# Kernel tuning notes

Measured on AMD Instinct MI355X. Metric: run time of the kernel, lower is better.

## Reference

```python
import jax, jax.numpy as jnp
import numpy as np
from jax import lax

K = 3  # kernel size
KK = K * K


def _bilinear_gather(img, ys, xs):
    """img: [C, H, W]; ys, xs: [KK, H, W] float sample coords.
    Returns [C, KK, H, W], zero outside the image (torch DCN zero-pad semantics)."""
    C, H, W = img.shape
    y0 = jnp.floor(ys).astype(jnp.int32)
    x0 = jnp.floor(xs).astype(jnp.int32)
    y1, x1 = y0 + 1, x0 + 1
    wy1 = ys - y0.astype(ys.dtype)
    wx1 = xs - x0.astype(xs.dtype)
    wy0, wx0 = 1.0 - wy1, 1.0 - wx1

    def g(yi, xi):
        valid = ((yi >= 0) & (yi < H) & (xi >= 0) & (xi < W)).astype(img.dtype)
        yc = jnp.clip(yi, 0, H - 1)
        xc = jnp.clip(xi, 0, W - 1)
        return img[:, yc, xc] * valid[None]  # [C, KK, H, W]

    return (wy0 * wx0) * g(y0, x0) + (wy0 * wx1) * g(y0, x1) \
         + (wy1 * wx0) * g(y1, x0) + (wy1 * wx1) * g(y1, x1)


def _df_layer(x, w_off, b_off, w):
    """One DFConv2d (modulated DCN, k=3, s=1, d=1, pad=1, groups=1) + ReLU."""
    B, C, H, W = x.shape
    O = w.shape[0]
    # offset/mask conv (standard 3x3, pad 1, with bias)
    om = lax.conv_general_dilated(x, w_off, (1, 1), [(1, 1), (1, 1)],
                                  dimension_numbers=('NCHW', 'OIHW', 'NCHW'))
    om = om + b_off[None, :, None, None]                     # [B, 27, H, W]
    off = om[:, :2 * KK].reshape(B, KK, 2, H, W)             # (dy, dx) per kernel pt
    mask = jax.nn.sigmoid(om[:, 2 * KK:3 * KK])              # [B, KK, H, W]

    ki, kj = jnp.meshgrid(jnp.arange(K), jnp.arange(K), indexing='ij')
    # base sampling grid: y = h - pad + i*dil = h + i - 1
    base_y = jnp.arange(H, dtype=x.dtype)[None, :, None] + (ki.reshape(KK, 1, 1).astype(x.dtype) - 1.0)
    base_x = jnp.arange(W, dtype=x.dtype)[None, None, :] + (kj.reshape(KK, 1, 1).astype(x.dtype) - 1.0)
    ys = base_y + off[:, :, 0]                               # [B, KK, H, W]
    xs = base_x + off[:, :, 1]

    sampled = jax.vmap(_bilinear_gather)(x, ys, xs)          # [B, C, KK, H, W]
    out = jnp.einsum('oik,bikhw->bohw', w.reshape(O, C, KK), sampled * mask[:, None])
    return jax.nn.relu(out)


def setup_inputs() -> dict:
    key = jax.random.key(0)
    ks = jax.random.split(key, 7)
    s = 0.05
    return {
        'x': jax.random.normal(ks[0], (2, 256, 96, 96), dtype=jnp.float32),
        'w_off0': jax.random.normal(ks[1], (27, 256, 3, 3), dtype=jnp.float32) * s,
        'b_off0': jnp.zeros((27,), dtype=jnp.float32),
        'w0': jax.random.normal(ks[2], (256, 256, 3, 3), dtype=jnp.float32) * s,
        'w_off1': jax.random.normal(ks[3], (27, 256, 3, 3), dtype=jnp.float32) * s,
        'b_off1': jnp.zeros((27,), dtype=jnp.float32),
        'w1': jax.random.normal(ks[4], (256, 256, 3, 3), dtype=jnp.float32) * s,
    }


def reference(x, w_off0, b_off0, w0, w_off1, b_off1, w1):
    h = _df_layer(x, w_off0, b_off0, w0)
    h = _df_layer(h, w_off1, b_off1, w1)
    return h
```

## Files before the change

### kernel.cpp

```cpp
#include <hip/hip_runtime.h>
#include <cstdint>
#include <cstddef>


#define KTOT 2304
#define PXB  9216

typedef __attribute__((ext_vector_type(8))) short bf16x8;
typedef __attribute__((ext_vector_type(4))) float f32x4;

static __device__ __forceinline__ unsigned short f2bf(float f) {
    union { float f; unsigned int u; } v; v.f = f;
    unsigned int r = (v.u + 0x7FFFu + ((v.u >> 16) & 1u)) >> 16;
    return (unsigned short)r;
}
static __device__ __forceinline__ float bf2f(unsigned short h) {
    union { unsigned int u; float f; } v; v.u = ((unsigned int)h) << 16;
    return v.f;
}
static __device__ __forceinline__ void unpack8(uint4 u, float* f) {
    union { unsigned int u; float f; } t;
    t.u = u.x << 16;         f[0] = t.f;
    t.u = u.x & 0xffff0000u; f[1] = t.f;
    t.u = u.y << 16;         f[2] = t.f;
    t.u = u.y & 0xffff0000u; f[3] = t.f;
    t.u = u.z << 16;         f[4] = t.f;
    t.u = u.z & 0xffff0000u; f[5] = t.f;
    t.u = u.w << 16;         f[6] = t.f;
    t.u = u.w & 0xffff0000u; f[7] = t.f;
}

__global__ __launch_bounds__(256) void transpose_kernel(const float* __restrict__ in,
                                                        unsigned short* __restrict__ outH,
                                                        unsigned short* __restrict__ outL) {
    __shared__ float tile[64][65];
    const int hw0 = blockIdx.x * 64;
    const int c0  = blockIdx.y * 64;
    const int b   = blockIdx.z;
    const int lx  = threadIdx.x & 63;
    const int ly  = threadIdx.x >> 6;
#pragma unroll
    for (int i = 0; i < 16; ++i) {
        int cl = ly + i * 4;
        tile[cl][lx] = in[(size_t)(b * 256 + c0 + cl) * PXB + hw0 + lx];
    }
    __syncthreads();
#pragma unroll
    for (int i = 0; i < 16; ++i) {
        int hwl = ly + i * 4;
        float v = tile[lx][hwl];
        size_t oi = ((size_t)b * PXB + hw0 + hwl) * 256 + c0 + lx;
        unsigned short hi = f2bf(v);
        outH[oi] = hi;
        outL[oi] = f2bf(v - bf2f(hi));
    }
}

__global__ __launch_bounds__(256) void prep_w_kernel(const float* __restrict__ w,
                                                     unsigned short* __restrict__ wA) {
    int idx = blockIdx.x * 256 + threadIdx.x;
    int o = idx / KTOT;
    int k = idx - o * KTOT;
    int kk = k >> 8;
    int c  = k & 255;
    wA[idx] = f2bf(w[o * KTOT + c * 9 + kk]);
}

__global__ __launch_bounds__(256) void prep_woff_kernel(const float* __restrict__ w,
                                                        unsigned short* __restrict__ wH,
                                                        unsigned short* __restrict__ wL) {
    int idx = blockIdx.x * 256 + threadIdx.x;
    int o = idx / KTOT;
    int k = idx - o * KTOT;
    int kk = k >> 8;
    int c  = k & 255;
    float f = (o < 27) ? w[o * KTOT + c * 9 + kk] : 0.0f;
    unsigned short hi = f2bf(f);
    wH[idx] = hi;
    wL[idx] = f2bf(f - bf2f(hi));
}

__global__ __launch_bounds__(512) void offconv_fused(const unsigned short* __restrict__ xH,
                                                     const unsigned short* __restrict__ xL,
                                                     const unsigned short* __restrict__ AH,
                                                     const unsigned short* __restrict__ AL,
                                                     const float* __restrict__ bias,
                                                     float* __restrict__ om) {
    __shared__ __attribute__((aligned(16))) unsigned short AsH[2][32 * 72];
    __shared__ __attribute__((aligned(16))) unsigned short AsL[2][32 * 72];
    __shared__ __attribute__((aligned(16))) unsigned short BsH[2][64 * 72];
    __shared__ __attribute__((aligned(16))) unsigned short BsL[2][64 * 72];

    const int tid  = threadIdx.x;
    const int kg   = tid >> 8;
    const int tl   = tid & 255;
    const int lane = tid & 63;
    const int wq   = (tid >> 6) & 3;
    const int quad = lane >> 4, l16 = lane & 15;
    const int g    = blockIdx.x;
    const int nb   = (g & 7) * 36 + (g >> 3);
    const int n0   = nb * 64;
    const int b    = n0 / PXB;
    const int hw0  = n0 - b * PXB;

    f32x4 acc[2];
#pragma unroll
    for (int mt = 0; mt < 2; ++mt) acc[mt] = (f32x4)0.0f;

    const int arow = tl >> 3, akg = tl & 7;

    uint4 pAH, pAL, pBH0, pBL0, pBH1, pBL1;
    auto pf = [&](int it) {
        const int kt = kg * 18 + it;
        const int kk = kt >> 2, c0 = (kt & 3) * 64;
        const int dy = kk / 3 - 1, dx = kk - (kk / 3) * 3 - 1;
        size_t ai = (size_t)arow * KTOT + kt * 64 + akg * 8;
        pAH = *(const uint4*)&AH[ai];
        pAL = *(const uint4*)&AL[ai];
#pragma unroll
        for (int i = 0; i < 2; ++i) {
            int task = i * 256 + tl;
            int px = task >> 3, cg = task & 7;
            int hw = hw0 + px;
            int h = hw / 96, w = hw - h * 96;
            int y = h + dy, x = w + dx;
            uint4 hv = make_uint4(0u, 0u, 0u, 0u), lv = make_uint4(0u, 0u, 0u, 0u);
            if (((unsigned)y < 96u) && ((unsigned)x < 96u)) {
                size_t bi = ((size_t)b * PXB + y * 96 + x) * 256 + c0 + cg * 8;
                hv = *(const uint4*)&xH[bi];
                lv = *(const uint4*)&xL[bi];
            }
            if (i == 0) { pBH0 = hv; pBL0 = lv; } else { pBH1 = hv; pBL1 = lv; }
        }
    };
    pf(0);

    for (int it = 0; it < 18; ++it) {
        __syncthreads();
        *(uint4*)&AsH[kg][arow * 72 + akg * 8] = pAH;
        *(uint4*)&AsL[kg][arow * 72 + akg * 8] = pAL;
        {
            int px = tl >> 3, cg = tl & 7;
            *(uint4*)&BsH[kg][px * 72 + cg * 8] = pBH0;
            *(uint4*)&BsL[kg][px * 72 + cg * 8] = pBL0;
        }
        {
            int task = 256 + tl;
            int px = task >> 3, cg = task & 7;
            *(uint4*)&BsH[kg][px * 72 + cg * 8] = pBH1;
            *(uint4*)&BsL[kg][px * 72 + cg * 8] = pBL1;
        }
        if (it < 17) pf(it + 1);
        __syncthreads();
#pragma unroll
        for (int ks = 0; ks < 2; ++ks) {
            bf16x8 ah[2], al[2], bh, bl;
#pragma unroll
            for (int mt = 0; mt < 2; ++mt) {
                ah[mt] = *(const bf16x8*)&AsH[kg][(mt * 16 + l16) * 72 + ks * 32 + quad * 8];
                al[mt] = *(const bf16x8*)&AsL[kg][(mt * 16 + l16) * 72 + ks * 32 + quad * 8];
            }
            bh = *(const bf16x8*)&BsH[kg][(wq * 16 + l16) * 72 + ks * 32 + quad * 8];
            bl = *(const bf16x8*)&BsL[kg][(wq * 16 + l16) * 72 + ks * 32 + quad * 8];
#pragma unroll
            for (int mt = 0; mt < 2; ++mt) {
                acc[mt] = __builtin_amdgcn_mfma_f32_16x16x32_bf16(ah[mt], bh, acc[mt], 0, 0, 0);
                acc[mt] = __builtin_amdgcn_mfma_f32_16x16x32_bf16(ah[mt], bl, acc[mt], 0, 0, 0);
                acc[mt] = __builtin_amdgcn_mfma_f32_16x16x32_bf16(al[mt], bh, acc[mt], 0, 0, 0);
            }
        }
    }

    float* red = (float*)BsH;
    __syncthreads();
    if (kg == 1) {
#pragma unroll
        for (int mt = 0; mt < 2; ++mt)
#pragma unroll
            for (int r = 0; r < 4; ++r)
                red[wq * 512 + mt * 256 + quad * 64 + r * 16 + l16] = acc[mt][r];
    }
    __syncthreads();
    if (kg == 0) {
#pragma unroll
        for (int mt = 0; mt < 2; ++mt)
#pragma unroll
            for (int r = 0; r < 4; ++r) {
                float v = acc[mt][r] + red[wq * 512 + mt * 256 + quad * 64 + r * 16 + l16];
                int m = mt * 16 + quad * 4 + r;
                int n = wq * 16 + l16;
                if (m < 27)
                    om[(size_t)(b * 27 + m) * PXB + hw0 + n] = v + bias[m];
            }
    }
}

__global__ __launch_bounds__(512, 4) void dfconv_v2(const unsigned short* __restrict__ xB,
                                                    const float* __restrict__ om,
                                                    const unsigned short* __restrict__ A,
                                                    float* __restrict__ out,
                                                    unsigned short* __restrict__ outH,
                                                    unsigned short* __restrict__ outL,
                                                    int out_mode) {
    __shared__ __attribute__((aligned(16))) char smem[48896];
    unsigned short* Bbuf0 = (unsigned short*)(smem + 32768);
    unsigned short* Bbuf1 = (unsigned short*)(smem + 37376);
    unsigned short* goff  = (unsigned short*)(smem + 41984);
    float*          gwt   = (float*)(smem + 44288);

    const int tid  = threadIdx.x;
    const int wv   = tid >> 6;
    const int lane = tid & 63;
    const int quad = lane >> 4, l16 = lane & 15;
    const int g    = blockIdx.x;
    const int nb   = (g & 7) * 72 + (g >> 3);
    const int n0   = nb * 32;
    const int b    = n0 / PXB;
    const int hw0  = n0 - b * PXB;

    if (tid < 288) {
        int task = tid;
        int px = task / 9;
        int kk = task - px * 9;
        int hw = hw0 + px;
        int h = hw / 96, w = hw - h * 96;
        const float* omp = om + (size_t)b * 27 * PXB + hw;
        float dyv = omp[(size_t)(2 * kk) * PXB];
        float dxv = omp[(size_t)(2 * kk + 1) * PXB];
        float mv  = omp[(size_t)(18 + kk) * PXB];
        float mk  = 1.0f / (1.0f + __expf(-mv));

        float ys = (float)(h + (kk / 3) - 1) + dyv;
        float xs = (float)(w + (kk - (kk / 3) * 3) - 1) + dxv;
        float fy = floorf(ys), fx = floorf(xs);
        int iy = (int)fy, ix = (int)fx;
        float wy1 = ys - fy, wx1 = xs - fx;
        float wy0 = 1.0f - wy1, wx0 = 1.0f - wx1;
        bool yv0 = (unsigned)iy < 96u, yv1 = (unsigned)(iy + 1) < 96u;
        bool xv0 = (unsigned)ix < 96u, xv1 = (unsigned)(ix + 1) < 96u;
        int y0 = min(max(iy, 0), 95),     y1 = min(max(iy + 1, 0), 95);
        int x0 = min(max(ix, 0), 95),     x1 = min(max(ix + 1, 0), 95);
        int gg = task * 4;
        goff[gg + 0] = (unsigned short)(y0 * 96 + x0);
        goff[gg + 1] = (unsigned short)(y0 * 96 + x1);
        goff[gg + 2] = (unsigned short)(y1 * 96 + x0);
        goff[gg + 3] = (unsigned short)(y1 * 96 + x1);
        gwt[gg + 0] = (yv0 && xv0) ? mk * wy0 * wx0 : 0.0f;
        gwt[gg + 1] = (yv0 && xv1) ? mk * wy0 * wx1 : 0.0f;
        gwt[gg + 2] = (yv1 && xv0) ? mk * wy1 * wx0 : 0.0f;
        gwt[gg + 3] = (yv1 && xv1) ? mk * wy1 * wx1 : 0.0f;
    }
    __syncthreads();

    const int px = (tid & 255) >> 3;
    const int cg = tid & 7;
    const unsigned short* xbase = xB + (size_t)b * PXB * 256 + cg * 8;

    const int arl = lane >> 3;
    const int akg = (lane & 7) ^ arl;

    f32x4 acc[2][2];
#pragma unroll
    for (int mt = 0; mt < 2; ++mt)
#pragma unroll
        for (int nt = 0; nt < 2; ++nt) acc[mt][nt] = (f32x4)0.0f;

    auto dmaA = [&](int kt) {
#pragma unroll
        for (int s = 0; s < 4; ++s) {
            const unsigned short* src =
                A + (size_t)(wv * 32 + s * 8 + arl) * KTOT + kt * 64 + akg * 8;
            char* dst = smem + wv * 4096 + s * 1024;
            __builtin_amdgcn_global_load_lds(
                (const __attribute__((address_space(1))) unsigned int*)src,
                (__attribute__((address_space(3))) unsigned int*)dst, 16, 0, 0);
        }
    };

    dmaA(0);
    if (tid < 256) {
        int gg = (px * 9 + 0) * 4;
        ushort4 o4 = *(const ushort4*)&goff[gg];
        float4 wt = *(const float4*)&gwt[gg];
        uint4 u0 = *(const uint4*)(xbase + (size_t)o4.x * 256);
        uint4 u1 = *(const uint4*)(xbase + (size_t)o4.y * 256);
        uint4 u2 = *(const uint4*)(xbase + (size_t)o4.z * 256);
        uint4 u3 = *(const uint4*)(xbase + (size_t)o4.w * 256);
        float f0[8], f1[8], f2[8], f3[8];
        unpack8(u0, f0); unpack8(u1, f1); unpack8(u2, f2); unpack8(u3, f3);
        unsigned short res[8];
#pragma unroll
        for (int j = 0; j < 8; ++j)
            res[j] = f2bf(wt.x * f0[j] + wt.y * f1[j] + wt.z * f2[j] + wt.w * f3[j]);
        *(uint4*)&Bbuf0[px * 72 + cg * 8] = *(uint4*)res;
    }
    __syncthreads();

    for (int r = 0; r < 36; ++r) {
        const int cur = r & 1;

        uint4 cc0, cc1, cc2, cc3; float4 wt;
        if (tid < 256 && r < 35) {
            const int ktn = r + 1, tap = ktn >> 2, c0 = (ktn & 3) * 64;
            int gg = (px * 9 + tap) * 4;
            ushort4 o4 = *(const ushort4*)&goff[gg];
            wt = *(const float4*)&gwt[gg];
            const unsigned short* cb = xbase + c0;
            cc0 = *(const uint4*)(cb + (size_t)o4.x * 256);
            cc1 = *(const uint4*)(cb + (size_t)o4.y * 256);
            cc2 = *(const uint4*)(cb + (size_t)o4.z * 256);
            cc3 = *(const uint4*)(cb + (size_t)o4.w * 256);
        }

        bf16x8 af00, af01, af10, af11;
        {
            const char* Ac = smem + wv * 4096;
            const int sw0 = ((quad ^ (l16 & 7)) * 16);
            const int sw1 = (((4 + quad) ^ (l16 & 7)) * 16);
            af00 = *(const bf16x8*)(Ac + l16 * 128 + sw0);
            af01 = *(const bf16x8*)(Ac + (16 + l16) * 128 + sw0);
            af10 = *(const bf16x8*)(Ac + l16 * 128 + sw1);
            af11 = *(const bf16x8*)(Ac + (16 + l16) * 128 + sw1);
        }
        asm volatile("s_waitcnt lgkmcnt(0)" ::: "memory");
        __builtin_amdgcn_sched_barrier(0);

        if (r < 35) dmaA(r + 1);

        {
            const unsigned short* Br = cur ? Bbuf1 : Bbuf0;
            bf16x8 b0 = *(const bf16x8*)&Br[l16 * 72 + quad * 8];
            bf16x8 b1 = *(const bf16x8*)&Br[(16 + l16) * 72 + quad * 8];
            acc[0][0] = __builtin_amdgcn_mfma_f32_16x16x32_bf16(af00, b0, acc[0][0], 0, 0, 0);
            acc[0][1] = __builtin_amdgcn_mfma_f32_16x16x32_bf16(af00, b1, acc[0][1], 0, 0, 0);
            acc[1][0] = __builtin_amdgcn_mfma_f32_16x16x32_bf16(af01, b0, acc[1][0], 0, 0, 0);
            acc[1][1] = __builtin_amdgcn_mfma_f32_16x16x32_bf16(af01, b1, acc[1][1], 0, 0, 0);
            bf16x8 b2 = *(const bf16x8*)&Br[l16 * 72 + 32 + quad * 8];
            bf16x8 b3 = *(const bf16x8*)&Br[(16 + l16) * 72 + 32 + quad * 8];
            acc[0][0] = __builtin_amdgcn_mfma_f32_16x16x32_bf16(af10, b2, acc[0][0], 0, 0, 0);
            acc[0][1] = __builtin_amdgcn_mfma_f32_16x16x32_bf16(af10, b3, acc[0][1], 0, 0, 0);
            acc[1][0] = __builtin_amdgcn_mfma_f32_16x16x32_bf16(af11, b2, acc[1][0], 0, 0, 0);
            acc[1][1] = __builtin_amdgcn_mfma_f32_16x16x32_bf16(af11, b3, acc[1][1], 0, 0, 0);
        }

        if (tid < 256 && r < 35) {
            unsigned short* Bw = cur ? Bbuf0 : Bbuf1;
            float f0[8], f1[8], f2[8], f3[8];
            unpack8(cc0, f0); unpack8(cc1, f1); unpack8(cc2, f2); unpack8(cc3, f3);
            unsigned short res[8];
#pragma unroll
            for (int j = 0; j < 8; ++j)
                res[j] = f2bf(wt.x * f0[j] + wt.y * f1[j] + wt.z * f2[j] + wt.w * f3[j]);
            *(uint4*)&Bw[px * 72 + cg * 8] = *(uint4*)res;
        }

        __syncthreads();
    }

    float* tileS = (float*)smem;
    if (out_mode == 0) {
#pragma unroll
        for (int pass = 0; pass < 2; ++pass) {
            if ((wv >> 2) == pass) {
#pragma unroll
                for (int mt = 0; mt < 2; ++mt)
#pragma unroll
                    for (int nt = 0; nt < 2; ++nt)
#pragma unroll
                        for (int rr = 0; rr < 4; ++rr) {
                            int ml = (wv & 3) * 32 + mt * 16 + quad * 4 + rr;
                            int n  = nt * 16 + l16;
                            tileS[ml * 36 + n] = fmaxf(acc[mt][nt][rr], 0.0f);
                        }
            }
            __syncthreads();
#pragma unroll
            for (int j = 0; j < 2; ++j) {
                int idx = j * 512 + tid;
                int row = idx >> 3, q = idx & 7;
                *(float4*)&out[(size_t)(b * 256 + pass * 128 + row) * PXB + hw0 + q * 4] =
                    *(const float4*)&tileS[row * 36 + q * 4];
            }
            __syncthreads();
        }
    } else {
#pragma unroll
        for (int pass = 0; pass < 2; ++pass) {
#pragma unroll
            for (int mt = 0; mt < 2; ++mt) {
                f32x4 v = acc[mt][pass];
                v[0] = fmaxf(v[0], 0.f); v[1] = fmaxf(v[1], 0.f);
                v[2] = fmaxf(v[2], 0.f); v[3] = fmaxf(v[3], 0.f);
                *(f32x4*)&tileS[l16 * 264 + wv * 32 + mt * 16 + quad * 4] = v;
            }
            __syncthreads();
#pragma unroll
            for (int j = 0; j < 2; ++j) {
                int idx = j * 512 + tid;
                int pxl = idx >> 6, ln = idx & 63;
                float4 v = *(const float4*)&tileS[pxl * 264 + ln * 4];
                size_t oi = ((size_t)b * PXB + hw0 + pass * 16 + pxl) * 256 + ln * 4;
                unsigned short hv[4], lv[4];
#pragma unroll
                for (int e = 0; e < 4; ++e) {
                    float fe = (e == 0) ? v.x : (e == 1) ? v.y : (e == 2) ? v.z : v.w;
                    hv[e] = f2bf(fe);
                    lv[e] = f2bf(fe - bf2f(hv[e]));
                }
                *(ushort4*)&outH[oi] = *(ushort4*)hv;
                *(ushort4*)&outL[oi] = *(ushort4*)lv;
            }
            __syncthreads();
        }
    }
}

extern "C" void kernel_launch(void* const* d_in, const int* in_sizes, int n_in,
                              void* d_out, int out_size, void* d_ws, size_t ws_size,
                              hipStream_t stream) {
    const float* x     = (const float*)d_in[0];
    const float* woff0 = (const float*)d_in[1];
    const float* boff0 = (const float*)d_in[2];
    const float* w0    = (const float*)d_in[3];
    const float* woff1 = (const float*)d_in[4];
    const float* boff1 = (const float*)d_in[5];
    const float* w1    = (const float*)d_in[6];
    float* out = (float*)d_out;

    char* p = (char*)d_ws;
    float* om  = (float*)p;  p += (size_t)2 * 27 * PXB * 4;
    unsigned short* xh  = (unsigned short*)p; p += (size_t)2 * 256 * PXB * 2;
    unsigned short* xl  = (unsigned short*)p; p += (size_t)2 * 256 * PXB * 2;
    unsigned short* h1h = (unsigned short*)p; p += (size_t)2 * 256 * PXB * 2;
    unsigned short* h1l = (unsigned short*)p; p += (size_t)2 * 256 * PXB * 2;
    unsigned short* wA0 = (unsigned short*)p; p += (size_t)256 * KTOT * 2;
    unsigned short* wA1 = (unsigned short*)p; p += (size_t)256 * KTOT * 2;
    unsigned short* wH0 = (unsigned short*)p; p += (size_t)32 * KTOT * 2;
    unsigned short* wL0 = (unsigned short*)p; p += (size_t)32 * KTOT * 2;
    unsigned short* wH1 = (unsigned short*)p; p += (size_t)32 * KTOT * 2;
    unsigned short* wL1 = (unsigned short*)p; p += (size_t)32 * KTOT * 2;

    hipLaunchKernelGGL(transpose_kernel, dim3(PXB / 64, 4, 2), dim3(256), 0, stream, x, xh, xl);
    hipLaunchKernelGGL(prep_w_kernel, dim3(256 * KTOT / 256), dim3(256), 0, stream, w0, wA0);
    hipLaunchKernelGGL(prep_w_kernel, dim3(256 * KTOT / 256), dim3(256), 0, stream, w1, wA1);
    hipLaunchKernelGGL(prep_woff_kernel, dim3(32 * KTOT / 256), dim3(256), 0, stream, woff0, wH0, wL0);
    hipLaunchKernelGGL(prep_woff_kernel, dim3(32 * KTOT / 256), dim3(256), 0, stream, woff1, wH1, wL1);

    hipLaunchKernelGGL(offconv_fused, dim3(288), dim3(512), 0, stream, xh, xl, wH0, wL0, boff0, om);
    hipLaunchKernelGGL(dfconv_v2, dim3(576), dim3(512), 0, stream, xh, om, wA0,
                       (float*)nullptr, h1h, h1l, 1);

    hipLaunchKernelGGL(offconv_fused, dim3(288), dim3(512), 0, stream, h1h, h1l, wH1, wL1, boff1, om);
    hipLaunchKernelGGL(dfconv_v2, dim3(576), dim3(512), 0, stream, h1h, om, wA1,
                       out, (unsigned short*)nullptr, (unsigned short*)nullptr, 0);
}
```

Baseline: 306.5 us.

## Widen deformable conv pixel tile to 64 so all threads gather and reuse A

Doubles the pixel tile per block from 32 to 64 and halves the grid to 288 blocks. All 512 threads now take part in the bilinear gather instead of only 256, and each A-weight tile loaded into LDS feeds twice as many MFMAs. This halves the total weight traffic and idle threads, but uses more LDS per block and twice the accumulator registers. With 288 blocks the grid is about one wave on 256 CUs, which may leave some CUs underused.

```diff
diff --git a/kernel.cpp b/kernel.cpp
--- a/kernel.cpp
+++ b/kernel.cpp
@@ -195,31 +195,29 @@
     }
 }
 
-__global__ __launch_bounds__(512, 4) void dfconv_v2(const unsigned short* __restrict__ xB,
+__global__ __launch_bounds__(512, 4) void dfconv_v4(const unsigned short* __restrict__ xB,
                                                     const float* __restrict__ om,
                                                     const unsigned short* __restrict__ A,
                                                     float* __restrict__ out,
                                                     unsigned short* __restrict__ outH,
                                                     unsigned short* __restrict__ outL,
                                                     int out_mode) {
-    __shared__ __attribute__((aligned(16))) char smem[48896];
-    unsigned short* Bbuf0 = (unsigned short*)(smem + 32768);
-    unsigned short* Bbuf1 = (unsigned short*)(smem + 37376);
-    unsigned short* goff  = (unsigned short*)(smem + 41984);
-    float*          gwt   = (float*)(smem + 44288);
+    __shared__ __attribute__((aligned(16))) char smem[65024];
+    unsigned short* BsD  = (unsigned short*)(smem + 32768);
+    unsigned short* goff = (unsigned short*)(smem + 51200);
+    float*          gwt  = (float*)(smem + 55808);
 
     const int tid  = threadIdx.x;
     const int wv   = tid >> 6;
     const int lane = tid & 63;
     const int quad = lane >> 4, l16 = lane & 15;
     const int g    = blockIdx.x;
-    const int nb   = (g & 7) * 72 + (g >> 3);
-    const int n0   = nb * 32;
+    const int nb   = (g & 7) * 36 + (g >> 3);
+    const int n0   = nb * 64;
     const int b    = n0 / PXB;
     const int hw0  = n0 - b * PXB;
 
-    if (tid < 288) {
-        int task = tid;
+    for (int task = tid; task < 576; task += 512) {
         int px = task / 9;
         int kk = task - px * 9;
         int hw = hw0 + px;
@@ -252,18 +250,18 @@
     }
     __syncthreads();
 
-    const int px = (tid & 255) >> 3;
+    const int px = tid >> 3;
     const int cg = tid & 7;
     const unsigned short* xbase = xB + (size_t)b * PXB * 256 + cg * 8;
 
     const int arl = lane >> 3;
     const int akg = (lane & 7) ^ arl;
 
-    f32x4 acc[2][2];
+    f32x4 acc[2][4];
 #pragma unroll
     for (int mt = 0; mt < 2; ++mt)
 #pragma unroll
-        for (int nt = 0; nt < 2; ++nt) acc[mt][nt] = (f32x4)0.0f;
+        for (int nt = 0; nt < 4; ++nt) acc[mt][nt] = (f32x4)0.0f;
 
     auto dmaA = [&](int kt) {
 #pragma unroll
@@ -278,7 +276,7 @@
     };
 
     dmaA(0);
-    if (tid < 256) {
+    {
         int gg = (px * 9 + 0) * 4;
         ushort4 o4 = *(const ushort4*)&goff[gg];
         float4 wt = *(const float4*)&gwt[gg];
@@ -292,7 +290,7 @@
 #pragma unroll
         for (int j = 0; j < 8; ++j)
             res[j] = f2bf(wt.x * f0[j] + wt.y * f1[j] + wt.z * f2[j] + wt.w * f3[j]);
-        *(uint4*)&Bbuf0[px * 72 + cg * 8] = *(uint4*)res;
+        *(uint4*)&BsD[px * 72 + cg * 8] = *(uint4*)res;
     }
     __syncthreads();
 
@@ -300,7 +298,7 @@
         const int cur = r & 1;
 
         uint4 cc0, cc1, cc2, cc3; float4 wt;
-        if (tid < 256 && r < 35) {
+        if (r < 35) {
             const int ktn = r + 1, tap = ktn >> 2, c0 = (ktn & 3) * 64;
             int gg = (px * 9 + tap) * 4;
             ushort4 o4 = *(const ushort4*)&goff[gg];
@@ -328,23 +326,23 @@
         if (r < 35) dmaA(r + 1);
 
         {
-            const unsigned short* Br = cur ? Bbuf1 : Bbuf0;
-            bf16x8 b0 = *(const bf16x8*)&Br[l16 * 72 + quad * 8];
-            bf16x8 b1 = *(const bf16x8*)&Br[(16 + l16) * 72 + quad * 8];
-            acc[0][0] = __builtin_amdgcn_mfma_f32_16x16x32_bf16(af00, b0, acc[0][0], 0, 0, 0);
-            acc[0][1] = __builtin_amdgcn_mfma_f32_16x16x32_bf16(af00, b1, acc[0][1], 0, 0, 0);
-            acc[1][0] = __builtin_amdgcn_mfma_f32_16x16x32_bf16(af01, b0, acc[1][0], 0, 0, 0);
-            acc[1][1] = __builtin_amdgcn_mfma_f32_16x16x32_bf16(af01, b1, acc[1][1], 0, 0, 0);
-            bf16x8 b2 = *(const bf16x8*)&Br[l16 * 72 + 32 + quad * 8];
-            bf16x8 b3 = *(const bf16x8*)&Br[(16 + l16) * 72 + 32 + quad * 8];
-            acc[0][0] = __builtin_amdgcn_mfma_f32_16x16x32_bf16(af10, b2, acc[0][0], 0, 0, 0);
-            acc[0][1] = __builtin_amdgcn_mfma_f32_16x16x32_bf16(af10, b3, acc[0][1], 0, 0, 0);
-            acc[1][0] = __builtin_amdgcn_mfma_f32_16x16x32_bf16(af11, b2, acc[1][0], 0, 0, 0);
-            acc[1][1] = __builtin_amdgcn_mfma_f32_16x16x32_bf16(af11, b3, acc[1][1], 0, 0, 0);
-        }
-
-        if (tid < 256 && r < 35) {
-            unsigned short* Bw = cur ? Bbuf0 : Bbuf1;
+            const unsigned short* Br = BsD + cur * 4608;
+#pragma unroll
+            for (int nt = 0; nt < 4; ++nt) {
+                bf16x8 b0 = *(const bf16x8*)&Br[(nt * 16 + l16) * 72 + quad * 8];
+                acc[0][nt] = __builtin_amdgcn_mfma_f32_16x16x32_bf16(af00, b0, acc[0][nt], 0, 0, 0);
+                acc[1][nt] = __builtin_amdgcn_mfma_f32_16x16x32_bf16(af01, b0, acc[1][nt], 0, 0, 0);
+            }
+#pragma unroll
+            for (int nt = 0; nt < 4; ++nt) {
+                bf16x8 b1 = *(const bf16x8*)&Br[(nt * 16 + l16) * 72 + 32 + quad * 8];
+                acc[0][nt] = __builtin_amdgcn_mfma_f32_16x16x32_bf16(af10, b1, acc[0][nt], 0, 0, 0);
+                acc[1][nt] = __builtin_amdgcn_mfma_f32_16x16x32_bf16(af11, b1, acc[1][nt], 0, 0, 0);
+            }
+        }
+
+        if (r < 35) {
+            unsigned short* Bw = BsD + (cur ^ 1) * 4608;
             float f0[8], f1[8], f2[8], f3[8];
             unpack8(cc0, f0); unpack8(cc1, f1); unpack8(cc2, f2); unpack8(cc3, f3);
             unsigned short res[8];
@@ -360,32 +358,32 @@
     float* tileS = (float*)smem;
     if (out_mode == 0) {
 #pragma unroll
-        for (int pass = 0; pass < 2; ++pass) {
-            if ((wv >> 2) == pass) {
+        for (int pass = 0; pass < 4; ++pass) {
+            if ((wv >> 1) == pass) {
 #pragma unroll
                 for (int mt = 0; mt < 2; ++mt)
 #pragma unroll
-                    for (int nt = 0; nt < 2; ++nt)
+                    for (int nt = 0; nt < 4; ++nt)
 #pragma unroll
                         for (int rr = 0; rr < 4; ++rr) {
-                            int ml = (wv & 3) * 32 + mt * 16 + quad * 4 + rr;
+                            int ml = (wv & 1) * 32 + mt * 16 + quad * 4 + rr;
                             int n  = nt * 16 + l16;
-                            tileS[ml * 36 + n] = fmaxf(acc[mt][nt][rr], 0.0f);
+                            tileS[ml * 68 + n] = fmaxf(acc[mt][nt][rr], 0.0f);
                         }
             }
             __syncthreads();
 #pragma unroll
             for (int j = 0; j < 2; ++j) {
                 int idx = j * 512 + tid;
-                int row = idx >> 3, q = idx & 7;
-                *(float4*)&out[(size_t)(b * 256 + pass * 128 + row) * PXB + hw0 + q * 4] =
-                    *(const float4*)&tileS[row * 36 + q * 4];
+                int row = idx >> 4, q = idx & 15;
+                *(float4*)&out[(size_t)(b * 256 + pass * 64 + row) * PXB + hw0 + q * 4] =
+                    *(const float4*)&tileS[row * 68 + q * 4];
             }
             __syncthreads();
         }
     } else {
 #pragma unroll
-        for (int pass = 0; pass < 2; ++pass) {
+        for (int pass = 0; pass < 4; ++pass) {
 #pragma unroll
             for (int mt = 0; mt < 2; ++mt) {
                 f32x4 v = acc[mt][pass];
@@ -447,10 +445,10 @@
     hipLaunchKernelGGL(prep_woff_kernel, dim3(32 * KTOT / 256), dim3(256), 0, stream, woff1, wH1, wL1);
 
     hipLaunchKernelGGL(offconv_fused, dim3(288), dim3(512), 0, stream, xh, xl, wH0, wL0, boff0, om);
-    hipLaunchKernelGGL(dfconv_v2, dim3(576), dim3(512), 0, stream, xh, om, wA0,
+    hipLaunchKernelGGL(dfconv_v4, dim3(288), dim3(512), 0, stream, xh, om, wA0,
                        (float*)nullptr, h1h, h1l, 1);
 
     hipLaunchKernelGGL(offconv_fused, dim3(288), dim3(512), 0, stream, h1h, h1l, wH1, wL1, boff1, om);
-    hipLaunchKernelGGL(dfconv_v2, dim3(576), dim3(512), 0, stream, h1h, om, wA1,
+    hipLaunchKernelGGL(dfconv_v4, dim3(288), dim3(512), 0, stream, h1h, om, wA1,
                        out, (unsigned short*)nullptr, (unsigned short*)nullptr, 0);
 }
```

New measurement: 316.4 us. 1.03x slower.
